# Kernel optimization log

Hardware: AMD Instinct MI355X
Metric: run time of the kernel (lower is better)

Reference implementation:

```python
import jax, jax.numpy as jnp
import numpy as np
import math

IN_FEATURE = 4096
OUT_FEATURE = 11008

def setup_inputs() -> dict:
    key = jax.random.key(0)
    k1, k2 = jax.random.split(key)
    x = jax.random.normal(k1, (4, 2048, IN_FEATURE), dtype=jnp.float32)
    # int8 weights in [-128, 127]; keep as int8 (stored as int32 spec-wise but cast to int8 here)
    int8_weights = jax.random.randint(k2, (OUT_FEATURE, IN_FEATURE), -128, 128, dtype=jnp.int32).astype(jnp.int8)
    scaler = jnp.float32(1.0 / 128.0 / math.sqrt(IN_FEATURE))
    return {"x": x, "int8_weights": int8_weights, "scaler": scaler}

def reference(x, int8_weights, scaler):
    # Dequantize int8 weights to fp32, then dense matmul: y = x @ W^T
    fp_weights = int8_weights.astype(jnp.float32) * scaler  # [O, I]
    return jnp.einsum('bsi,oi->bso', x, fp_weights)
```

## Files before the change

### kernel.cpp

```cpp
#include <hip/hip_runtime.h>

typedef __attribute__((ext_vector_type(8))) short short8;
typedef __attribute__((ext_vector_type(8))) unsigned short ushort8;
typedef __attribute__((ext_vector_type(4))) float f32x4;
typedef __attribute__((ext_vector_type(4))) float float4v;
typedef __attribute__((ext_vector_type(4))) int int4v;

#define GLB_CAST(p) ((const __attribute__((address_space(1))) void*)(p))
#define LDS_CAST(p) ((__attribute__((address_space(3))) void*)(p))

__device__ __forceinline__ unsigned short f2bf_rne(float f) {
  unsigned u = __builtin_bit_cast(unsigned, f);
  u += 0x7fffu + ((u >> 16) & 1u);
  return (unsigned short)(u >> 16);
}

__device__ __forceinline__ bool w_looks_int32(const int* wi) {
  bool all_small = true;
#pragma unroll
  for (int i = 0; i < 16; ++i) {
    int v = wi[i];
    if (v > 127 || v < -128) all_small = false;
  }
  return all_small;
}


__global__ void pack_w_kernel(const void* __restrict__ w, int4v* __restrict__ wq, long n16) {
  const bool is32 = w_looks_int32((const int*)w);
  if (!is32) return;
  long stride = (long)gridDim.x * blockDim.x;
  for (long i = blockIdx.x * (long)blockDim.x + threadIdx.x; i < n16; i += stride) {
    const int4v* w4 = (const int4v*)w;
    int4v r;
#pragma unroll
    for (int qd = 0; qd < 4; ++qd) {
      int4v raw = w4[i * 4 + qd];
      r[qd] = (raw[0] & 0xff) | ((raw[1] & 0xff) << 8) | ((raw[2] & 0xff) << 16) | (raw[3] << 24);
    }
    wq[i] = r;
  }
}

__global__ __launch_bounds__(256) void rowquant_kernel(const float* __restrict__ x,
                                                       int* __restrict__ q,
                                                       float* __restrict__ rowscale, int K) {
  const int row = blockIdx.x;
  const int tid = threadIdx.x;
  const float4v* xr = (const float4v*)(x + (long)row * K);

  float4v v[4];
  float m = 0.f;
#pragma unroll
  for (int c = 0; c < 4; ++c) {
    v[c] = xr[c * 256 + tid];
#pragma unroll
    for (int j = 0; j < 4; ++j) m = fmaxf(m, fabsf(v[c][j]));
  }
#pragma unroll
  for (int off = 32; off >= 1; off >>= 1) m = fmaxf(m, __shfl_xor(m, off));
  __shared__ float wmax[4];
  if ((tid & 63) == 0) wmax[tid >> 6] = m;
  __syncthreads();
  m = fmaxf(fmaxf(wmax[0], wmax[1]), fmaxf(wmax[2], wmax[3]));

  const float k = (m > 0.f) ? 127.f / m : 0.f;
  int* qr = q + (long)row * (K >> 2);
#pragma unroll
  for (int c = 0; c < 4; ++c) {
    int wv_ = 0;
#pragma unroll
    for (int j = 0; j < 4; ++j) {
      int b = (int)__builtin_rintf(v[c][j] * k);
      wv_ |= (b & 0xff) << (8 * j);
    }
    qr[c * 256 + tid] = wv_;
  }
  if (tid == 0) rowscale[row] = m;
}

__global__ __launch_bounds__(512, 2) void gemm256_i8_kernel(
    const signed char* __restrict__ wraw, const signed char* __restrict__ wq,
    const signed char* __restrict__ A, float* __restrict__ C,
    const float* __restrict__ rowscale, const float* __restrict__ scaler,
    int M, int N, int K) {
  __shared__ __align__(16) char lds[131072];

  const signed char* Bw = w_looks_int32((const int*)wraw) ? wq : wraw;

  const int tid  = threadIdx.x;
  const int lane = tid & 63;
  const int wv   = tid >> 6;
  const int wm   = wv >> 2;
  const int wn   = wv & 3;
  const int fr   = lane & 15;
  const int fq   = lane >> 4;

  const int nwg  = gridDim.x;
  const int orig = blockIdx.x;
  const int ntn  = N >> 8;
  const int ntm  = M >> 8;
  int tm, tn;
  if (((nwg & 7) == 0) && ((ntm & 7) == 0)) {
    const int c     = orig & 7;
    const int w     = orig >> 3;
    const int bandh = ntm >> 3;
    tm = c * bandh + (w % bandh);
    tn = w / bandh;
  } else {
    tm = orig / ntn;
    tn = orig - tm * ntn;
  }
  const long rowBase = (long)tm << 8;
  const long colBase = (long)tn << 8;

  const int    srow  = tid >> 3;
  const int    scolb = (((tid & 7) ^ (srow & 7)) << 4);
  const size_t rowb  = (size_t)K;
  const size_t hstep = rowb << 7;
  const size_t r64   = rowb << 6;
  const char*  gA    = (const char*)A + (rowBase + srow) * rowb + scolb;
  const char*  gB    = (const char*)Bw + (colBase + srow) * rowb + scolb;
  const int    dst   = tid << 4;

#define STAGE(gsrc, loff)                                                                              \
  do {                                                                                                 \
    __builtin_amdgcn_global_load_lds(GLB_CAST(gsrc), LDS_CAST(lds + (loff) + dst), 16, 0, 0);          \
    __builtin_amdgcn_global_load_lds(GLB_CAST((gsrc) + r64), LDS_CAST(lds + (loff) + 8192 + dst), 16, 0, 0); \
  } while (0)

  int offA[4][2], offB[2][2];
#pragma unroll
  for (int i = 0; i < 4; ++i) {
    const int lr = i * 32 + wm * 16 + fr;
    const int sw = (lr & 7) << 4;
#pragma unroll
    for (int kk = 0; kk < 2; ++kk) offA[i][kk] = lr * 128 + ((kk * 64 + fq * 16) ^ sw);
  }
#pragma unroll
  for (int j = 0; j < 2; ++j) {
    const int lr = j * 64 + wn * 16 + fr;
    const int sw = (lr & 7) << 4;
#pragma unroll
    for (int kk = 0; kk < 2; ++kk) offB[j][kk] = lr * 128 + ((kk * 64 + fq * 16) ^ sw);
  }

  int4v acc[8][4] = {};
  int4v af[4][2], bf[4][2];
  const int nt = K >> 7;

  STAGE(gA,         0);
  STAGE(gB,         32768);
  STAGE(gA + hstep, 16384);
  STAGE(gB + hstep, 49152);
  asm volatile("s_waitcnt vmcnt(4)" ::: "memory");
  if (nt > 1) {
    STAGE(gA + 128,         65536);
    STAGE(gB + 128,         65536 + 32768);
    STAGE(gA + hstep + 128, 65536 + 16384);
  }
  asm volatile("s_waitcnt vmcnt(6)" ::: "memory");
  __builtin_amdgcn_s_barrier();

  for (int t = 0; t < nt; ++t) {
    const int cur = (t & 1) << 16;
    const int nxt = cur ^ 65536;
    const size_t kof1 = (size_t)(t + 1) << 7;
    const size_t kof2 = (size_t)(t + 2) << 7;

#pragma unroll
    for (int i = 0; i < 4; ++i) {
      af[i][0] = *(const int4v*)(lds + cur + offA[i][0]);
      af[i][1] = *(const int4v*)(lds + cur + offA[i][1]);
    }
#pragma unroll
    for (int j = 0; j < 2; ++j) {
      bf[j][0] = *(const int4v*)(lds + cur + 32768 + offB[j][0]);
      bf[j][1] = *(const int4v*)(lds + cur + 32768 + offB[j][1]);
    }
    if (t + 1 < nt) STAGE(gB + hstep + kof1, nxt + 49152);
    __builtin_amdgcn_s_barrier();
    __builtin_amdgcn_s_setprio(1);
#pragma unroll
    for (int i = 0; i < 4; ++i)
#pragma unroll
      for (int j = 0; j < 2; ++j) {
        acc[i][j] = __builtin_amdgcn_mfma_i32_16x16x64_i8(af[i][0], bf[j][0], acc[i][j], 0, 0, 0);
        acc[i][j] = __builtin_amdgcn_mfma_i32_16x16x64_i8(af[i][1], bf[j][1], acc[i][j], 0, 0, 0);
      }
    __builtin_amdgcn_s_setprio(0);
    __builtin_amdgcn_s_barrier();

#pragma unroll
    for (int j = 2; j < 4; ++j) {
      bf[j][0] = *(const int4v*)(lds + cur + 49152 + offB[j - 2][0]);
      bf[j][1] = *(const int4v*)(lds + cur + 49152 + offB[j - 2][1]);
    }
    if (t + 2 < nt) STAGE(gA + kof2, cur + 0);
    __builtin_amdgcn_s_barrier();
    __builtin_amdgcn_s_setprio(1);
#pragma unroll
    for (int i = 0; i < 4; ++i)
#pragma unroll
      for (int j = 2; j < 4; ++j) {
        acc[i][j] = __builtin_amdgcn_mfma_i32_16x16x64_i8(af[i][0], bf[j][0], acc[i][j], 0, 0, 0);
        acc[i][j] = __builtin_amdgcn_mfma_i32_16x16x64_i8(af[i][1], bf[j][1], acc[i][j], 0, 0, 0);
      }
    __builtin_amdgcn_s_setprio(0);
    __builtin_amdgcn_s_barrier();

#pragma unroll
    for (int i = 0; i < 4; ++i) {
      af[i][0] = *(const int4v*)(lds + cur + 16384 + offA[i][0]);
      af[i][1] = *(const int4v*)(lds + cur + 16384 + offA[i][1]);
    }
    if (t + 2 < nt) STAGE(gB + kof2, cur + 32768);
    __builtin_amdgcn_s_barrier();
    __builtin_amdgcn_s_setprio(1);
#pragma unroll
    for (int i = 0; i < 4; ++i)
#pragma unroll
      for (int j = 2; j < 4; ++j) {
        acc[4 + i][j] = __builtin_amdgcn_mfma_i32_16x16x64_i8(af[i][0], bf[j][0], acc[4 + i][j], 0, 0, 0);
        acc[4 + i][j] = __builtin_amdgcn_mfma_i32_16x16x64_i8(af[i][1], bf[j][1], acc[4 + i][j], 0, 0, 0);
      }
    __builtin_amdgcn_s_setprio(0);
    __builtin_amdgcn_s_barrier();

    if (t + 2 < nt) STAGE(gA + hstep + kof2, cur + 16384);
    __builtin_amdgcn_s_barrier();
    __builtin_amdgcn_s_setprio(1);
#pragma unroll
    for (int i = 0; i < 4; ++i)
#pragma unroll
      for (int j = 0; j < 2; ++j) {
        acc[4 + i][j] = __builtin_amdgcn_mfma_i32_16x16x64_i8(af[i][0], bf[j][0], acc[4 + i][j], 0, 0, 0);
        acc[4 + i][j] = __builtin_amdgcn_mfma_i32_16x16x64_i8(af[i][1], bf[j][1], acc[4 + i][j], 0, 0, 0);
      }
    __builtin_amdgcn_s_setprio(0);
    if (t + 2 < nt)      { asm volatile("s_waitcnt vmcnt(6)" ::: "memory"); }
    else if (t + 1 < nt) { asm volatile("s_waitcnt vmcnt(0)" ::: "memory"); }
    if (t + 1 < nt) __builtin_amdgcn_s_barrier();
  }
#undef STAGE

  const float s = (*scaler) * (1.f / 127.f);
#pragma unroll
  for (int mi = 0; mi < 8; ++mi) {
#pragma unroll
    for (int j = 0; j < 4; ++j) {
      const long row = rowBase + mi * 32 + wm * 16 + fq * 4 + j;
      const float sc = rowscale[row] * s;
      float* cp = C + row * (long)N + colBase + wn * 16 + fr;
#pragma unroll
      for (int nj = 0; nj < 4; ++nj) cp[(size_t)nj * 64] = (float)acc[mi][nj][j] * sc;
    }
  }
}


__global__ void cvt_x_kernel(const float* __restrict__ x, ushort8* __restrict__ xh, long n8) {
  long stride = (long)gridDim.x * blockDim.x;
  for (long i = blockIdx.x * (long)blockDim.x + threadIdx.x; i < n8; i += stride) {
    float4v a = reinterpret_cast<const float4v*>(x)[2 * i + 0];
    float4v b = reinterpret_cast<const float4v*>(x)[2 * i + 1];
    ushort8 r;
#pragma unroll
    for (int j = 0; j < 4; ++j) {
      r[j]     = f2bf_rne(a[j]);
      r[4 + j] = f2bf_rne(b[j]);
    }
    xh[i] = r;
  }
}

__global__ void cvt_w_kernel(const void* __restrict__ w, ushort8* __restrict__ wh,
                             const float* __restrict__ sp, long n16) {
  const float s = *sp;
  const bool is32 = w_looks_int32((const int*)w);
  long stride = (long)gridDim.x * blockDim.x;
  for (long i = blockIdx.x * (long)blockDim.x + threadIdx.x; i < n16; i += stride) {
    unsigned short tmp[16];
    if (is32) {
      const int4v* w4 = (const int4v*)w;
#pragma unroll
      for (int q = 0; q < 4; ++q) {
        int4v raw = w4[i * 4 + q];
#pragma unroll
        for (int j = 0; j < 4; ++j) tmp[4 * q + j] = f2bf_rne((float)raw[j] * s);
      }
    } else {
      int4v raw = reinterpret_cast<const int4v*>(w)[i];
#pragma unroll
      for (int q = 0; q < 4; ++q) {
        int v = raw[q];
        tmp[4 * q + 0] = f2bf_rne((float)(int)(signed char)(v & 0xff) * s);
        tmp[4 * q + 1] = f2bf_rne((float)(int)(signed char)((v >> 8) & 0xff) * s);
        tmp[4 * q + 2] = f2bf_rne((float)(int)(signed char)((v >> 16) & 0xff) * s);
        tmp[4 * q + 3] = f2bf_rne((float)(v >> 24) * s);
      }
    }
    ushort8 r0, r1;
#pragma unroll
    for (int j = 0; j < 8; ++j) { r0[j] = tmp[j]; r1[j] = tmp[8 + j]; }
    wh[2 * i + 0] = r0;
    wh[2 * i + 1] = r1;
  }
}

#define BM 128
#define BN 128
#define BK 32
__global__ __launch_bounds__(256) void gemm_bt_kernel(
    const unsigned short* __restrict__ A, const unsigned short* __restrict__ Bw,
    float* __restrict__ C, int M, int N, int K) {
  __shared__ __align__(16) unsigned short As[BM * BK];
  __shared__ __align__(16) unsigned short Bs[BN * BK];
  const int t = threadIdx.x, lane = t & 63, wv = t >> 6, wr = wv >> 1, wc = wv & 1;
  const long rowBase = (long)blockIdx.y * BM, colBase = (long)blockIdx.x * BN;
  const int r0 = t >> 2, cb0 = (t & 3) * 16, r1 = r0 + 64;
  const char* gA0 = (const char*)(A + (rowBase + r0) * (long)K) + cb0;
  const char* gA1 = (const char*)(A + (rowBase + r1) * (long)K) + cb0;
  const char* gB0 = (const char*)(Bw + (colBase + r0) * (long)K) + cb0;
  const char* gB1 = (const char*)(Bw + (colBase + r1) * (long)K) + cb0;
  char* lA0 = (char*)As + wv * 1024; char* lA1 = (char*)As + 4096 + wv * 1024;
  char* lB0 = (char*)Bs + wv * 1024; char* lB1 = (char*)Bs + 4096 + wv * 1024;
  const int fr = lane & 15, kb = (lane >> 4) * 16;
  const char* aBase = (const char*)As + (wr * 64 + fr) * (BK * 2) + kb;
  const char* bBase = (const char*)Bs + (wc * 64 + fr) * (BK * 2) + kb;
  f32x4 acc[4][4] = {};
  for (int k0 = 0; k0 < K; k0 += BK) {
    const long koff = (long)k0 * 2;
    __builtin_amdgcn_global_load_lds(GLB_CAST(gA0 + koff), LDS_CAST(lA0), 16, 0, 0);
    __builtin_amdgcn_global_load_lds(GLB_CAST(gA1 + koff), LDS_CAST(lA1), 16, 0, 0);
    __builtin_amdgcn_global_load_lds(GLB_CAST(gB0 + koff), LDS_CAST(lB0), 16, 0, 0);
    __builtin_amdgcn_global_load_lds(GLB_CAST(gB1 + koff), LDS_CAST(lB1), 16, 0, 0);
    __syncthreads();
    short8 af[4], bfv[4];
#pragma unroll
    for (int mi = 0; mi < 4; ++mi) af[mi] = *reinterpret_cast<const short8*>(aBase + mi * 16 * (BK * 2));
#pragma unroll
    for (int nj = 0; nj < 4; ++nj) bfv[nj] = *reinterpret_cast<const short8*>(bBase + nj * 16 * (BK * 2));
#pragma unroll
    for (int mi = 0; mi < 4; ++mi)
#pragma unroll
      for (int nj = 0; nj < 4; ++nj)
        acc[mi][nj] = __builtin_amdgcn_mfma_f32_16x16x32_bf16(af[mi], bfv[nj], acc[mi][nj], 0, 0, 0);
    __syncthreads();
  }
  const int fq = lane >> 4;
#pragma unroll
  for (int mi = 0; mi < 4; ++mi)
#pragma unroll
    for (int j = 0; j < 4; ++j) {
      const long row = rowBase + wr * 64 + mi * 16 + fq * 4 + j;
      float* cp = C + row * (long)N + colBase + wc * 64 + fr;
#pragma unroll
      for (int nj = 0; nj < 4; ++nj) cp[nj * 16] = acc[mi][nj][j];
    }
}

__global__ void gemm_naive_kernel(const float* __restrict__ x, const void* __restrict__ w,
                                  const float* __restrict__ sp, float* __restrict__ out,
                                  int M, int N, int K) {
  const bool is32 = w_looks_int32((const int*)w);
  int n = blockIdx.x * 16 + threadIdx.x;
  int m = blockIdx.y * 16 + threadIdx.y;
  if (m >= M || n >= N) return;
  const float* xr = x + (long)m * K;
  float acc = 0.f;
  if (is32) {
    const int* wr_ = (const int*)w + (long)n * K;
    for (int k = 0; k < K; ++k) acc += xr[k] * (float)wr_[k];
  } else {
    const signed char* wr_ = (const signed char*)w + (long)n * K;
    for (int k = 0; k < K; ++k) acc += xr[k] * (float)wr_[k];
  }
  out[(long)m * N + n] = acc * (*sp);
}

extern "C" void kernel_launch(void* const* d_in, const int* in_sizes, int n_in,
                              void* d_out, int out_size, void* d_ws, size_t ws_size,
                              hipStream_t stream) {
  const float* x      = (const float*)d_in[0];
  const void*  w      = (const void*)d_in[1];
  const float* scaler = (const float*)d_in[2];
  float*       out    = (float*)d_out;

  const int K = 4096;
  const int N = 11008;
  const int M = in_sizes[0] / K;

  const size_t xq_bytes = (size_t)M * K;
  const size_t wq_bytes = (size_t)N * K;
  const size_t rs_bytes = (size_t)M * 4;
  const size_t i8_need  = xq_bytes + wq_bytes + rs_bytes + 64;

  if ((M % 256 == 0) && (N % 256 == 0) && (K == 4096) && ws_size >= i8_need) {
    signed char* xq = (signed char*)d_ws;
    signed char* wq = (signed char*)((char*)d_ws + xq_bytes);
    float*       rs = (float*)((char*)d_ws + xq_bytes + wq_bytes);

    pack_w_kernel<<<512, 256, 0, stream>>>(w, (int4v*)wq, (long)N * K / 16);
    rowquant_kernel<<<M, 256, 0, stream>>>(x, (int*)xq, rs, K);
    gemm256_i8_kernel<<<dim3((M / 256) * (N / 256)), 512, 0, stream>>>(
        (const signed char*)w, wq, xq, out, rs, scaler, M, N, K);
    return;
  }

  const size_t xh_bytes = (size_t)M * K * 2;
  const size_t wh_bytes = (size_t)N * K * 2;
  if (ws_size < xh_bytes + wh_bytes) {
    dim3 g((N + 15) / 16, (M + 15) / 16), b(16, 16);
    gemm_naive_kernel<<<g, b, 0, stream>>>(x, w, scaler, out, M, N, K);
    return;
  }

  unsigned short* xh = (unsigned short*)d_ws;
  unsigned short* wh = (unsigned short*)((char*)d_ws + xh_bytes);
  cvt_x_kernel<<<2048, 256, 0, stream>>>(x, (ushort8*)xh, (long)M * K / 8);
  cvt_w_kernel<<<2048, 256, 0, stream>>>(w, (ushort8*)wh, scaler, (long)N * K / 16);
  gemm_bt_kernel<<<dim3(N / BN, M / BM), 256, 0, stream>>>(xh, wh, out, M, N, K);
}
```

Before: 473.9 us.

## Replace 256x256 pipelined int8 GEMM with simpler 128x128 single-buffered tile

```diff
diff --git a/kernel.cpp b/kernel.cpp
--- a/kernel.cpp
+++ b/kernel.cpp
@@ -79,27 +79,27 @@
   if (tid == 0) rowscale[row] = m;
 }
 
-__global__ __launch_bounds__(512, 2) void gemm256_i8_kernel(
+__global__ __launch_bounds__(256, 2) void gemm128_i8_kernel(
     const signed char* __restrict__ wraw, const signed char* __restrict__ wq,
     const signed char* __restrict__ A, float* __restrict__ C,
     const float* __restrict__ rowscale, const float* __restrict__ scaler,
     int M, int N, int K) {
-  __shared__ __align__(16) char lds[131072];
+  __shared__ __align__(16) char lds[32768];
 
   const signed char* Bw = w_looks_int32((const int*)wraw) ? wq : wraw;
 
   const int tid  = threadIdx.x;
   const int lane = tid & 63;
   const int wv   = tid >> 6;
-  const int wm   = wv >> 2;
-  const int wn   = wv & 3;
+  const int wm   = wv >> 1;
+  const int wn   = wv & 1;
   const int fr   = lane & 15;
   const int fq   = lane >> 4;
 
   const int nwg  = gridDim.x;
   const int orig = blockIdx.x;
-  const int ntn  = N >> 8;
-  const int ntm  = M >> 8;
+  const int ntn  = N >> 7;
+  const int ntm  = M >> 7;
   int tm, tn;
   if (((nwg & 7) == 0) && ((ntm & 7) == 0)) {
     const int c     = orig & 7;
@@ -111,149 +111,89 @@
     tm = orig / ntn;
     tn = orig - tm * ntn;
   }
-  const long rowBase = (long)tm << 8;
-  const long colBase = (long)tn << 8;
+  const long rowBase = (long)tm << 7;
+  const long colBase = (long)tn << 7;
 
   const int    srow  = tid >> 3;
   const int    scolb = (((tid & 7) ^ (srow & 7)) << 4);
   const size_t rowb  = (size_t)K;
-  const size_t hstep = rowb << 7;
-  const size_t r64   = rowb << 6;
+  const size_t r32   = rowb << 5;
   const char*  gA    = (const char*)A + (rowBase + srow) * rowb + scolb;
   const char*  gB    = (const char*)Bw + (colBase + srow) * rowb + scolb;
   const int    dst   = tid << 4;
 
-#define STAGE(gsrc, loff)                                                                              \
-  do {                                                                                                 \
-    __builtin_amdgcn_global_load_lds(GLB_CAST(gsrc), LDS_CAST(lds + (loff) + dst), 16, 0, 0);          \
-    __builtin_amdgcn_global_load_lds(GLB_CAST((gsrc) + r64), LDS_CAST(lds + (loff) + 8192 + dst), 16, 0, 0); \
+#define STAGE_TILE(koff)                                                                                \
+  do {                                                                                                  \
+    _Pragma("unroll") for (int s = 0; s < 4; ++s)                                                       \
+      __builtin_amdgcn_global_load_lds(GLB_CAST(gA + (koff) + s * r32),                                 \
+                                       LDS_CAST(lds + s * 4096 + dst), 16, 0, 0);                       \
+    _Pragma("unroll") for (int s = 0; s < 4; ++s)                                                       \
+      __builtin_amdgcn_global_load_lds(GLB_CAST(gB + (koff) + s * r32),                                 \
+                                       LDS_CAST(lds + 16384 + s * 4096 + dst), 16, 0, 0);               \
   } while (0)
 
-  int offA[4][2], offB[2][2];
+  int offA[4][2], offB[4][2];
 #pragma unroll
   for (int i = 0; i < 4; ++i) {
-    const int lr = i * 32 + wm * 16 + fr;
+    const int lr = wm * 64 + i * 16 + fr;
     const int sw = (lr & 7) << 4;
 #pragma unroll
     for (int kk = 0; kk < 2; ++kk) offA[i][kk] = lr * 128 + ((kk * 64 + fq * 16) ^ sw);
   }
 #pragma unroll
-  for (int j = 0; j < 2; ++j) {
-    const int lr = j * 64 + wn * 16 + fr;
+  for (int j = 0; j < 4; ++j) {
+    const int lr = wn * 64 + j * 16 + fr;
     const int sw = (lr & 7) << 4;
 #pragma unroll
     for (int kk = 0; kk < 2; ++kk) offB[j][kk] = lr * 128 + ((kk * 64 + fq * 16) ^ sw);
   }
 
-  int4v acc[8][4] = {};
+  int4v acc[4][4] = {};
   int4v af[4][2], bf[4][2];
   const int nt = K >> 7;
 
-  STAGE(gA,         0);
-  STAGE(gB,         32768);
-  STAGE(gA + hstep, 16384);
-  STAGE(gB + hstep, 49152);
-  asm volatile("s_waitcnt vmcnt(4)" ::: "memory");
-  if (nt > 1) {
-    STAGE(gA + 128,         65536);
-    STAGE(gB + 128,         65536 + 32768);
-    STAGE(gA + hstep + 128, 65536 + 16384);
-  }
-  asm volatile("s_waitcnt vmcnt(6)" ::: "memory");
-  __builtin_amdgcn_s_barrier();
+  STAGE_TILE(0);
+  __syncthreads();
 
   for (int t = 0; t < nt; ++t) {
-    const int cur = (t & 1) << 16;
-    const int nxt = cur ^ 65536;
-    const size_t kof1 = (size_t)(t + 1) << 7;
-    const size_t kof2 = (size_t)(t + 2) << 7;
-
 #pragma unroll
     for (int i = 0; i < 4; ++i) {
-      af[i][0] = *(const int4v*)(lds + cur + offA[i][0]);
-      af[i][1] = *(const int4v*)(lds + cur + offA[i][1]);
-    }
-#pragma unroll
-    for (int j = 0; j < 2; ++j) {
-      bf[j][0] = *(const int4v*)(lds + cur + 32768 + offB[j][0]);
-      bf[j][1] = *(const int4v*)(lds + cur + 32768 + offB[j][1]);
-    }
-    if (t + 1 < nt) STAGE(gB + hstep + kof1, nxt + 49152);
-    __builtin_amdgcn_s_barrier();
+      af[i][0] = *(const int4v*)(lds + offA[i][0]);
+      af[i][1] = *(const int4v*)(lds + offA[i][1]);
+    }
+#pragma unroll
+    for (int j = 0; j < 4; ++j) {
+      bf[j][0] = *(const int4v*)(lds + 16384 + offB[j][0]);
+      bf[j][1] = *(const int4v*)(lds + 16384 + offB[j][1]);
+    }
+    __syncthreads();
+
+    if (t + 1 < nt) STAGE_TILE((size_t)(t + 1) << 7);
+
     __builtin_amdgcn_s_setprio(1);
 #pragma unroll
     for (int i = 0; i < 4; ++i)
 #pragma unroll
-      for (int j = 0; j < 2; ++j) {
+      for (int j = 0; j < 4; ++j) {
         acc[i][j] = __builtin_amdgcn_mfma_i32_16x16x64_i8(af[i][0], bf[j][0], acc[i][j], 0, 0, 0);
         acc[i][j] = __builtin_amdgcn_mfma_i32_16x16x64_i8(af[i][1], bf[j][1], acc[i][j], 0, 0, 0);
       }
     __builtin_amdgcn_s_setprio(0);
-    __builtin_amdgcn_s_barrier();
-
-#pragma unroll
-    for (int j = 2; j < 4; ++j) {
-      bf[j][0] = *(const int4v*)(lds + cur + 49152 + offB[j - 2][0]);
-      bf[j][1] = *(const int4v*)(lds + cur + 49152 + offB[j - 2][1]);
-    }
-    if (t + 2 < nt) STAGE(gA + kof2, cur + 0);
-    __builtin_amdgcn_s_barrier();
-    __builtin_amdgcn_s_setprio(1);
-#pragma unroll
-    for (int i = 0; i < 4; ++i)
-#pragma unroll
-      for (int j = 2; j < 4; ++j) {
-        acc[i][j] = __builtin_amdgcn_mfma_i32_16x16x64_i8(af[i][0], bf[j][0], acc[i][j], 0, 0, 0);
-        acc[i][j] = __builtin_amdgcn_mfma_i32_16x16x64_i8(af[i][1], bf[j][1], acc[i][j], 0, 0, 0);
-      }
-    __builtin_amdgcn_s_setprio(0);
-    __builtin_amdgcn_s_barrier();
-
-#pragma unroll
-    for (int i = 0; i < 4; ++i) {
-      af[i][0] = *(const int4v*)(lds + cur + 16384 + offA[i][0]);
-      af[i][1] = *(const int4v*)(lds + cur + 16384 + offA[i][1]);
-    }
-    if (t + 2 < nt) STAGE(gB + kof2, cur + 32768);
-    __builtin_amdgcn_s_barrier();
-    __builtin_amdgcn_s_setprio(1);
-#pragma unroll
-    for (int i = 0; i < 4; ++i)
-#pragma unroll
-      for (int j = 2; j < 4; ++j) {
-        acc[4 + i][j] = __builtin_amdgcn_mfma_i32_16x16x64_i8(af[i][0], bf[j][0], acc[4 + i][j], 0, 0, 0);
-        acc[4 + i][j] = __builtin_amdgcn_mfma_i32_16x16x64_i8(af[i][1], bf[j][1], acc[4 + i][j], 0, 0, 0);
-      }
-    __builtin_amdgcn_s_setprio(0);
-    __builtin_amdgcn_s_barrier();
-
-    if (t + 2 < nt) STAGE(gA + hstep + kof2, cur + 16384);
-    __builtin_amdgcn_s_barrier();
-    __builtin_amdgcn_s_setprio(1);
-#pragma unroll
-    for (int i = 0; i < 4; ++i)
-#pragma unroll
-      for (int j = 0; j < 2; ++j) {
-        acc[4 + i][j] = __builtin_amdgcn_mfma_i32_16x16x64_i8(af[i][0], bf[j][0], acc[4 + i][j], 0, 0, 0);
-        acc[4 + i][j] = __builtin_amdgcn_mfma_i32_16x16x64_i8(af[i][1], bf[j][1], acc[4 + i][j], 0, 0, 0);
-      }
-    __builtin_amdgcn_s_setprio(0);
-    if (t + 2 < nt)      { asm volatile("s_waitcnt vmcnt(6)" ::: "memory"); }
-    else if (t + 1 < nt) { asm volatile("s_waitcnt vmcnt(0)" ::: "memory"); }
-    if (t + 1 < nt) __builtin_amdgcn_s_barrier();
-  }
-#undef STAGE
+
+    __syncthreads();
+  }
+#undef STAGE_TILE
 
   const float s = (*scaler) * (1.f / 127.f);
 #pragma unroll
-  for (int mi = 0; mi < 8; ++mi) {
-#pragma unroll
-    for (int j = 0; j < 4; ++j) {
-      const long row = rowBase + mi * 32 + wm * 16 + fq * 4 + j;
+  for (int i = 0; i < 4; ++i) {
+#pragma unroll
+    for (int jj = 0; jj < 4; ++jj) {
+      const long row = rowBase + wm * 64 + i * 16 + fq * 4 + jj;
       const float sc = rowscale[row] * s;
-      float* cp = C + row * (long)N + colBase + wn * 16 + fr;
-#pragma unroll
-      for (int nj = 0; nj < 4; ++nj) cp[(size_t)nj * 64] = (float)acc[mi][nj][j] * sc;
+      float* cp = C + row * (long)N + colBase + wn * 64 + fr;
+#pragma unroll
+      for (int j = 0; j < 4; ++j) cp[(size_t)j * 16] = (float)acc[i][j][jj] * sc;
     }
   }
 }
@@ -396,14 +336,14 @@
   const size_t rs_bytes = (size_t)M * 4;
   const size_t i8_need  = xq_bytes + wq_bytes + rs_bytes + 64;
 
-  if ((M % 256 == 0) && (N % 256 == 0) && (K == 4096) && ws_size >= i8_need) {
+  if ((M % 128 == 0) && (N % 128 == 0) && (K == 4096) && ws_size >= i8_need) {
     signed char* xq = (signed char*)d_ws;
     signed char* wq = (signed char*)((char*)d_ws + xq_bytes);
     float*       rs = (float*)((char*)d_ws + xq_bytes + wq_bytes);
 
     pack_w_kernel<<<512, 256, 0, stream>>>(w, (int4v*)wq, (long)N * K / 16);
     rowquant_kernel<<<M, 256, 0, stream>>>(x, (int*)xq, rs, K);
-    gemm256_i8_kernel<<<dim3((M / 256) * (N / 256)), 512, 0, stream>>>(
+    gemm128_i8_kernel<<<dim3((M / 128) * (N / 128)), 256, 0, stream>>>(
         (const signed char*)w, wq, xq, out, rs, scaler, M, N, K);
     return;
   }
```

New measurement: 473.6 us, median of 2. Within noise of the previous version (-0.1%).
